# Kernel tuning notes

Hardware: AMD Instinct MI355X
Metric: run time of the kernel (lower is better)

## Reference

```python
import jax, jax.numpy as jnp
import numpy as np

NEG_SLOPE = 0.2
EPS = 1e-16  # PyG softmax denominator epsilon


def _gatv2_layer(x, src, dst, n_nodes, W_l, W_r, att, bias):
    """Single-head GATv2Conv (PyG defaults, self loops already in src/dst).
    x: [N, F_in]; src/dst: [E]; W_l/W_r: [F_in, F_out]; att: [F_out]; bias: [F_out].
    """
    x_l = x @ W_l                       # source transform [N, F_out]
    x_r = x @ W_r                       # target transform [N, F_out]
    # per-edge attention logit: a^T LeakyReLU(x_l[j] + x_r[i])
    e = jax.nn.leaky_relu(x_l[src] + x_r[dst], NEG_SLOPE) @ att  # [E]
    # softmax over incoming edges of each destination node
    e_max = jax.ops.segment_max(e, dst, num_segments=n_nodes)    # [N]
    ex = jnp.exp(e - e_max[dst])                                  # [E]
    denom = jax.ops.segment_sum(ex, dst, num_segments=n_nodes)   # [N]
    alpha = ex / (denom[dst] + EPS)                               # [E]
    out = jax.ops.segment_sum(alpha[:, None] * x_l[src], dst, num_segments=n_nodes)
    return out + bias


def setup_inputs() -> dict:
    key = jax.random.key(0)
    N, E = 50000, 800000
    IN, HID, OUT = 128, 64, 64
    ks = jax.random.split(key, 12)
    x = jax.random.normal(ks[0], (N, IN), dtype=jnp.float32)
    edge_index = jax.random.randint(ks[1], (2, E), 0, N, dtype=jnp.int64)
    s1 = float(1.0 / np.sqrt(IN))
    s2 = float(1.0 / np.sqrt(HID))
    return {
        "x": x,
        "edge_index": edge_index,
        "W1_l": jax.random.uniform(ks[2], (IN, HID), jnp.float32, -s1, s1),
        "W1_r": jax.random.uniform(ks[3], (IN, HID), jnp.float32, -s1, s1),
        "att1": jax.random.uniform(ks[4], (HID,), jnp.float32, -s2, s2),
        "b1": jnp.zeros((HID,), jnp.float32),
        "W2_l": jax.random.uniform(ks[5], (HID, OUT), jnp.float32, -s2, s2),
        "W2_r": jax.random.uniform(ks[6], (HID, OUT), jnp.float32, -s2, s2),
        "att2": jax.random.uniform(ks[7], (OUT,), jnp.float32, -s2, s2),
        "b2": jnp.zeros((OUT,), jnp.float32),
    }


def reference(x, edge_index, W1_l, W1_r, att1, b1, W2_l, W2_r, att2, b2):
    n = x.shape[0]
    loop = jnp.arange(n, dtype=edge_index.dtype)
    src = jnp.concatenate([edge_index[0], loop])  # add self loops (PyG default)
    dst = jnp.concatenate([edge_index[1], loop])
    h = _gatv2_layer(x, src, dst, n, W1_l, W1_r, att1, b1)
    h = jax.nn.relu(h)
    out = _gatv2_layer(h, src, dst, n, W2_l, W2_r, att2, b2)
    return out
```

## Files before the change

kernel.cpp:

```cpp
#include <hip/hip_runtime.h>
#include <math.h>

#define NEG_SLOPE 0.2f
#define EPSV 1e-16f
#define NEG_HUGE -1e30f
#define CAP 64
#define GH 512

typedef short short8 __attribute__((ext_vector_type(8)));
typedef float f32x4 __attribute__((ext_vector_type(4)));
typedef unsigned short u16;


__device__ __forceinline__ u16 f2bf(float f) {
    const unsigned u = __float_as_uint(f);
    return (u16)((u + 0x7fffu + ((u >> 16) & 1u)) >> 16);
}
__device__ __forceinline__ float bf2f(u16 h) {
    return __uint_as_float(((unsigned)h) << 16);
}

__global__ __launch_bounds__(256) void k_wpack(
        const float* __restrict__ W1l, const float* __restrict__ W1r,
        const float* __restrict__ W2l, const float* __restrict__ W2r,
        u16* __restrict__ w1hi, u16* __restrict__ w1lo,
        u16* __restrict__ w2hi, u16* __restrict__ w2lo,
        int* __restrict__ cnt, u16* __restrict__ csrc, int N, int NP) {
    const int idx = blockIdx.x * 256 + threadIdx.x;
    const int G = gridDim.x * 256;
    const int CN = 8 * NP;
    for (int i = idx; i < CN; i += G) {
        const int cls = i / NP;
        const int r = i - cls * NP;
        const int d = r * 8 + cls;
        cnt[i] = (d < N) ? 1 : 0;
    }
    for (int d = idx; d < N; d += G) csrc[(size_t)d * CAP] = (u16)d;
    const int T1 = 128 * 128, T2 = 64 * 128;
    if (idx >= T1 + T2) return;
    u16 *dhi, *dlo; const float *Wl, *Wr; int li;
    if (idx < T1) { dhi = w1hi; dlo = w1lo; Wl = W1l; Wr = W1r; li = idx; }
    else          { dhi = w2hi; dlo = w2lo; Wl = W2l; Wr = W2r; li = idx - T1; }
    const int j = li & 7, l = (li >> 3) & 63, t = (li >> 9) & 7, c = li >> 12;
    const int k = c * 32 + (l >> 4) * 8 + j;
    const int n = t * 16 + (l & 15);
    const float v = (n < 64) ? Wl[k * 64 + n] : Wr[k * 64 + (n - 64)];
    const unsigned u = __float_as_uint(v);
    dhi[li] = (u16)(u >> 16);
    const float hif = __uint_as_float(u & 0xffff0000u);
    dlo[li] = (u16)(__float_as_uint(v - hif) >> 16);
}

__device__ __forceinline__ void split8(const float* fs, short8& ahi, short8& alo) {
#pragma unroll
    for (int j = 0; j < 8; ++j) {
        const unsigned u = __float_as_uint(fs[j]);
        ahi[j] = (short)(u >> 16);
        const float hif = __uint_as_float(u & 0xffff0000u);
        alo[j] = (short)(__float_as_uint(fs[j] - hif) >> 16);
    }
}

template <int K>
__device__ __forceinline__ void gemm_mfma_tile(const float* __restrict__ X,
                                               const u16* __restrict__ whi,
                                               const u16* __restrict__ wlo,
                                               u16* __restrict__ xl,
                                               float* __restrict__ xr,
                                               int N, int tile) {
    const int lane = threadIdx.x & 63;
    const int w = threadIdx.x >> 6;
    const int rowbase = tile * 64 + w * 16;
    const int m = lane & 15, q = lane >> 4;
    int ar = rowbase + m; if (ar > N - 1) ar = N - 1;
    const float* arow = X + (size_t)ar * K + q * 8;
    f32x4 acc[8];
#pragma unroll
    for (int t = 0; t < 8; ++t) acc[t] = (f32x4){0.f, 0.f, 0.f, 0.f};
#pragma unroll
    for (int c = 0; c < K / 32; ++c) {
        const float4 f0 = *(const float4*)(arow + c * 32);
        const float4 f1 = *(const float4*)(arow + c * 32 + 4);
        const float fs[8] = {f0.x, f0.y, f0.z, f0.w, f1.x, f1.y, f1.z, f1.w};
        short8 ahi, alo;
        split8(fs, ahi, alo);
        const u16* bp = whi + ((size_t)(c * 8) * 64 + lane) * 8;
        const u16* bq = wlo + ((size_t)(c * 8) * 64 + lane) * 8;
#pragma unroll
        for (int t = 0; t < 8; ++t) {
            const short8 bhi = *(const short8*)(bp + t * 64 * 8);
            const short8 blo = *(const short8*)(bq + t * 64 * 8);
            acc[t] = __builtin_amdgcn_mfma_f32_16x16x32_bf16(bhi, ahi, acc[t], 0, 0, 0);
            acc[t] = __builtin_amdgcn_mfma_f32_16x16x32_bf16(blo, ahi, acc[t], 0, 0, 0);
            acc[t] = __builtin_amdgcn_mfma_f32_16x16x32_bf16(bhi, alo, acc[t], 0, 0, 0);
        }
    }
    const int row = rowbase + m;
    if (row < N) {
#pragma unroll
        for (int t = 0; t < 8; ++t) {
            const int colb = t * 16 + q * 4;
            if (t < 4) {
                ushort4 hv;
                hv.x = f2bf(acc[t][0]); hv.y = f2bf(acc[t][1]);
                hv.z = f2bf(acc[t][2]); hv.w = f2bf(acc[t][3]);
                *(ushort4*)(xl + (size_t)row * 64 + colb) = hv;
            } else {
                float4 v;
                v.x = acc[t][0]; v.y = acc[t][1]; v.z = acc[t][2]; v.w = acc[t][3];
                *(float4*)(xr + (size_t)row * 64 + (colb - 64)) = v;
            }
        }
    }
}

template <int K>
__global__ __launch_bounds__(256) void k_hist_gemm(const int* __restrict__ ei, int E,
                                                   int* __restrict__ cnt,
                                                   u16* __restrict__ csrc,
                                                   const float* __restrict__ X,
                                                   const u16* __restrict__ whi,
                                                   const u16* __restrict__ wlo,
                                                   u16* __restrict__ xl,
                                                   float* __restrict__ xr,
                                                   int N, int NP) {
    if ((int)blockIdx.x < GH) {
        const int cls = blockIdx.x & 7;
        const int stripe = blockIdx.x >> 3;
        const int NS = GH >> 3;
        const int tid = threadIdx.x;
        const int* srcp = ei;
        const int* dstp = ei + E;
        int* cntc = cnt + cls * NP;
        if ((E & 3) == 0) {
            for (int base = stripe * 1024; base < E; base += NS * 1024) {
                const int e4 = base + tid * 4;
                if (e4 < E) {
                    const int4 d4 = *(const int4*)(dstp + e4);
                    const int4 s4 = *(const int4*)(srcp + e4);
                    const int d[4] = {d4.x, d4.y, d4.z, d4.w};
                    const int s[4] = {s4.x, s4.y, s4.z, s4.w};
                    bool m[4]; int sl[4];
#pragma unroll
                    for (int j = 0; j < 4; ++j) {
                        m[j] = (d[j] & 7) == cls;
                        if (m[j]) sl[j] = atomicAdd(&cntc[d[j] >> 3], 1);
                    }
#pragma unroll
                    for (int j = 0; j < 4; ++j) {
                        if (m[j]) csrc[(size_t)d[j] * CAP + sl[j]] = (u16)s[j];
                    }
                }
            }
        } else {
            for (int base = stripe * 256; base < E; base += NS * 256) {
                const int e = base + tid;
                if (e < E) {
                    const int dd = dstp[e];
                    if ((dd & 7) == cls) {
                        const int ss = srcp[e];
                        const int slot = atomicAdd(&cntc[dd >> 3], 1);
                        csrc[(size_t)dd * CAP + slot] = (u16)ss;
                    }
                }
            }
        }
    } else {
        gemm_mfma_tile<K>(X, whi, wlo, xl, xr, N, blockIdx.x - GH);
    }
}

template <int K>
__global__ __launch_bounds__(256) void k_gemm(const float* __restrict__ X,
                                              const u16* __restrict__ whi,
                                              const u16* __restrict__ wlo,
                                              u16* __restrict__ xl,
                                              float* __restrict__ xr, int N) {
    gemm_mfma_tile<K>(X, whi, wlo, xl, xr, N, blockIdx.x);
}

template <int NT>
__device__ __forceinline__ void attn_core(const u16* __restrict__ xl,
                                          int sidx, int deg, int base,
                                          int g, int i,
                                          const float4 xrv, const float4 aw,
                                          float& l, float4& acc) {
    ushort4 u[NT][4];
    bool vv[NT][4];
#pragma unroll
    for (int nt = 0; nt < NT; ++nt) {
#pragma unroll
        for (int j = 0; j < 4; ++j) {
            const int s = base + nt * 16 + j * 4 + g;
            vv[nt][j] = s < deg;
            const int src = __shfl(sidx, s, 64);
            u[nt][j] = *(const ushort4*)(xl + (size_t)src * 64 + i * 4);
        }
    }
#pragma unroll
    for (int nt = 0; nt < NT; ++nt) {
#pragma unroll
        for (int j = 0; j < 4; ++j) {
            float4 va;
            va.x = bf2f(u[nt][j].x); va.y = bf2f(u[nt][j].y);
            va.z = bf2f(u[nt][j].z); va.w = bf2f(u[nt][j].w);
            float t0, pp;
            t0 = va.x + xrv.x; t0 = fmaxf(t0, NEG_SLOPE * t0); pp = aw.x * t0;
            t0 = va.y + xrv.y; t0 = fmaxf(t0, NEG_SLOPE * t0); pp = fmaf(aw.y, t0, pp);
            t0 = va.z + xrv.z; t0 = fmaxf(t0, NEG_SLOPE * t0); pp = fmaf(aw.z, t0, pp);
            t0 = va.w + xrv.w; t0 = fmaxf(t0, NEG_SLOPE * t0); pp = fmaf(aw.w, t0, pp);
            pp += __shfl_xor(pp, 1, 64);
            pp += __shfl_xor(pp, 2, 64);
            pp += __shfl_xor(pp, 4, 64);
            pp += __shfl_xor(pp, 8, 64);
            const float dj = __expf(vv[nt][j] ? pp : NEG_HUGE);
            l += dj;
            acc.x = fmaf(dj, va.x, acc.x);
            acc.y = fmaf(dj, va.y, acc.y);
            acc.z = fmaf(dj, va.z, acc.z);
            acc.w = fmaf(dj, va.w, acc.w);
        }
    }
}

__global__ __launch_bounds__(256) void k_attn(const u16* __restrict__ xl,
                                              const float* xr,
                                              const float* __restrict__ att,
                                              const int* __restrict__ cnt,
                                              const u16* __restrict__ csrc,
                                              const float* __restrict__ bias,
                                              float* out, int N, int NP, int relu) {
    const int lane = threadIdx.x & 63;
    const int g = lane >> 4;
    const int i = lane & 15;
    const int dst = blockIdx.x * 4 + (threadIdx.x >> 6);
    if (dst >= N) return;
    const float4 xrv = *(const float4*)(xr + (size_t)dst * 64 + i * 4);
    const float4 aw  = *(const float4*)(att + i * 4);
    const int deg = cnt[(dst & 7) * NP + (dst >> 3)];
    const int sidx = (int)csrc[(size_t)dst * CAP + ((lane < deg) ? lane : 0)];
    float l = 0.0f;
    float4 acc = {0.0f, 0.0f, 0.0f, 0.0f};
    if (deg <= 16) {
        attn_core<1>(xl, sidx, deg, 0, g, i, xrv, aw, l, acc);
    } else if (deg <= 32) {
        attn_core<2>(xl, sidx, deg, 0, g, i, xrv, aw, l, acc);
    } else {
        attn_core<2>(xl, sidx, deg, 0, g, i, xrv, aw, l, acc);
        attn_core<2>(xl, sidx, deg, 32, g, i, xrv, aw, l, acc);
    }
#pragma unroll
    for (int o = 16; o <= 32; o <<= 1) {
        l     += __shfl_xor(l, o, 64);
        acc.x += __shfl_xor(acc.x, o, 64);
        acc.y += __shfl_xor(acc.y, o, 64);
        acc.z += __shfl_xor(acc.z, o, 64);
        acc.w += __shfl_xor(acc.w, o, 64);
    }
    if (g == 0) {
        const float4 bv = *(const float4*)(bias + i * 4);
        const float inv = 1.0f / (l + EPSV);
        float4 r;
        r.x = fmaf(acc.x, inv, bv.x);
        r.y = fmaf(acc.y, inv, bv.y);
        r.z = fmaf(acc.z, inv, bv.z);
        r.w = fmaf(acc.w, inv, bv.w);
        if (relu) {
            r.x = fmaxf(r.x, 0.0f); r.y = fmaxf(r.y, 0.0f);
            r.z = fmaxf(r.z, 0.0f); r.w = fmaxf(r.w, 0.0f);
        }
        *(float4*)(out + (size_t)dst * 64 + i * 4) = r;
    }
}


extern "C" void kernel_launch(void* const* d_in, const int* in_sizes, int n_in,
                              void* d_out, int out_size, void* d_ws, size_t ws_size,
                              hipStream_t stream) {
    const float* x    = (const float*)d_in[0];
    const int*   ei   = (const int*)d_in[1];
    const float* W1l  = (const float*)d_in[2];
    const float* W1r  = (const float*)d_in[3];
    const float* att1 = (const float*)d_in[4];
    const float* b1   = (const float*)d_in[5];
    const float* W2l  = (const float*)d_in[6];
    const float* W2r  = (const float*)d_in[7];
    const float* att2 = (const float*)d_in[8];
    const float* b2   = (const float*)d_in[9];

    const int N  = in_sizes[0] / 128;
    const int E  = in_sizes[1] / 2;
    const int NP = (((N + 7) >> 3) + 31) & ~31;

    int* wsi   = (int*)d_ws;
    int* cnt   = wsi;
    u16* csrc  = (u16*)(cnt + 8 * NP);
    u16* w1hi  = csrc + (size_t)N * CAP;
    u16* w1lo  = w1hi + 16384;
    u16* w2hi  = w1lo + 16384;
    u16* w2lo  = w2hi + 8192;
    float* buf1 = (float*)(w2lo + 8192);
    float* buf2 = buf1 + (size_t)N * 64;
    float* fout = (float*)d_out;

    const dim3 b256(256);
    const int gGemm = (N + 63) / 64;
    const int gAttn = (N + 3) / 4;

    k_wpack<<<96, b256, 0, stream>>>(
        W1l, W1r, W2l, W2r, w1hi, w1lo, w2hi, w2lo, cnt, csrc, N, NP);

    k_hist_gemm<128><<<GH + gGemm, b256, 0, stream>>>(ei, E, cnt, csrc,
                                                      x, w1hi, w1lo,
                                                      (u16*)fout, buf1, N, NP);
    k_attn<<<gAttn, b256, 0, stream>>>((const u16*)fout, buf1, att1, cnt, csrc, b1,
                                       buf2, N, NP, 1);

    k_gemm<64><<<gGemm, b256, 0, stream>>>(buf2, w2hi, w2lo, (u16*)buf1, fout, N);
    k_attn<<<gAttn, b256, 0, stream>>>((const u16*)buf1, fout, att2, cnt, csrc, b2,
                                       fout, N, NP, 0);
}
```

Before: 206.9 us.

## Fuse layer-1 attention with layer-2 GEMM via shared-memory row tiles

Layer-1 attention and the layer-2 projection GEMM now run in one kernel. Each block computes 16 hidden rows into shared memory, then one wave multiplies them by W2 using split-bf16 MFMA and writes xl2/xr2 directly. This removes a kernel launch and the global round trip of the hidden activations. In exchange, only one of four waves does the GEMM while the others idle, and each wave now handles four destinations in sequence, which may cut memory-level parallelism in the gather phase.

```diff
diff --git a/kernel.cpp b/kernel.cpp
--- a/kernel.cpp
+++ b/kernel.cpp
@@ -170,15 +170,6 @@
     }
 }
 
-template <int K>
-__global__ __launch_bounds__(256) void k_gemm(const float* __restrict__ X,
-                                              const u16* __restrict__ whi,
-                                              const u16* __restrict__ wlo,
-                                              u16* __restrict__ xl,
-                                              float* __restrict__ xr, int N) {
-    gemm_mfma_tile<K>(X, whi, wlo, xl, xr, N, blockIdx.x);
-}
-
 template <int NT>
 __device__ __forceinline__ void attn_core(const u16* __restrict__ xl,
                                           int sidx, int deg, int base,
@@ -223,20 +214,15 @@
     }
 }
 
-__global__ __launch_bounds__(256) void k_attn(const u16* __restrict__ xl,
-                                              const float* xr,
-                                              const float* __restrict__ att,
-                                              const int* __restrict__ cnt,
-                                              const u16* __restrict__ csrc,
-                                              const float* __restrict__ bias,
-                                              float* out, int N, int NP, int relu) {
-    const int lane = threadIdx.x & 63;
-    const int g = lane >> 4;
-    const int i = lane & 15;
-    const int dst = blockIdx.x * 4 + (threadIdx.x >> 6);
-    if (dst >= N) return;
+__device__ __forceinline__ float4 attn_row(const u16* __restrict__ xl,
+                                           const float* __restrict__ xr,
+                                           const float4 aw,
+                                           const int* __restrict__ cnt,
+                                           const u16* __restrict__ csrc,
+                                           const float* __restrict__ bias,
+                                           int dst, int NP, int relu,
+                                           int lane, int g, int i) {
     const float4 xrv = *(const float4*)(xr + (size_t)dst * 64 + i * 4);
-    const float4 aw  = *(const float4*)(att + i * 4);
     const int deg = cnt[(dst & 7) * NP + (dst >> 3)];
     const int sidx = (int)csrc[(size_t)dst * CAP + ((lane < deg) ? lane : 0)];
     float l = 0.0f;
@@ -257,20 +243,103 @@
         acc.z += __shfl_xor(acc.z, o, 64);
         acc.w += __shfl_xor(acc.w, o, 64);
     }
-    if (g == 0) {
-        const float4 bv = *(const float4*)(bias + i * 4);
-        const float inv = 1.0f / (l + EPSV);
-        float4 r;
-        r.x = fmaf(acc.x, inv, bv.x);
-        r.y = fmaf(acc.y, inv, bv.y);
-        r.z = fmaf(acc.z, inv, bv.z);
-        r.w = fmaf(acc.w, inv, bv.w);
-        if (relu) {
-            r.x = fmaxf(r.x, 0.0f); r.y = fmaxf(r.y, 0.0f);
-            r.z = fmaxf(r.z, 0.0f); r.w = fmaxf(r.w, 0.0f);
-        }
+    const float4 bv = *(const float4*)(bias + i * 4);
+    const float inv = 1.0f / (l + EPSV);
+    float4 r;
+    r.x = fmaf(acc.x, inv, bv.x);
+    r.y = fmaf(acc.y, inv, bv.y);
+    r.z = fmaf(acc.z, inv, bv.z);
+    r.w = fmaf(acc.w, inv, bv.w);
+    if (relu) {
+        r.x = fmaxf(r.x, 0.0f); r.y = fmaxf(r.y, 0.0f);
+        r.z = fmaxf(r.z, 0.0f); r.w = fmaxf(r.w, 0.0f);
+    }
+    return r;
+}
+
+__global__ __launch_bounds__(256) void k_attn1_gemm2(
+        const u16* __restrict__ xl, const float* __restrict__ xr,
+        const float* __restrict__ att, const int* __restrict__ cnt,
+        const u16* __restrict__ csrc, const float* __restrict__ bias,
+        const u16* __restrict__ w2hi, const u16* __restrict__ w2lo,
+        u16* __restrict__ xl2, float* __restrict__ xr2, int N, int NP) {
+    __shared__ float hrow[16][68];
+    const int lane = threadIdx.x & 63;
+    const int wv = threadIdx.x >> 6;
+    const int g = lane >> 4;
+    const int i = lane & 15;
+    const int rowbase = blockIdx.x * 16;
+    const float4 aw = *(const float4*)(att + i * 4);
+    for (int p = 0; p < 4; ++p) {
+        const int dst = rowbase + wv * 4 + p;
+        if (dst < N) {
+            const float4 r = attn_row(xl, xr, aw, cnt, csrc, bias,
+                                      dst, NP, 1, lane, g, i);
+            if (g == 0) *(float4*)&hrow[wv * 4 + p][i * 4] = r;
+        }
+    }
+    __syncthreads();
+    if (wv != 0) return;
+    const int m = lane & 15, q = lane >> 4;
+    const float* arow = &hrow[m][0] + q * 8;
+    f32x4 acc[8];
+#pragma unroll
+    for (int t = 0; t < 8; ++t) acc[t] = (f32x4){0.f, 0.f, 0.f, 0.f};
+#pragma unroll
+    for (int c = 0; c < 2; ++c) {
+        const float4 f0 = *(const float4*)(arow + c * 32);
+        const float4 f1 = *(const float4*)(arow + c * 32 + 4);
+        const float fs[8] = {f0.x, f0.y, f0.z, f0.w, f1.x, f1.y, f1.z, f1.w};
+        short8 ahi, alo;
+        split8(fs, ahi, alo);
+        const u16* bp = w2hi + ((size_t)(c * 8) * 64 + lane) * 8;
+        const u16* bq = w2lo + ((size_t)(c * 8) * 64 + lane) * 8;
+#pragma unroll
+        for (int t = 0; t < 8; ++t) {
+            const short8 bhi = *(const short8*)(bp + t * 64 * 8);
+            const short8 blo = *(const short8*)(bq + t * 64 * 8);
+            acc[t] = __builtin_amdgcn_mfma_f32_16x16x32_bf16(bhi, ahi, acc[t], 0, 0, 0);
+            acc[t] = __builtin_amdgcn_mfma_f32_16x16x32_bf16(blo, ahi, acc[t], 0, 0, 0);
+            acc[t] = __builtin_amdgcn_mfma_f32_16x16x32_bf16(bhi, alo, acc[t], 0, 0, 0);
+        }
+    }
+    const int row = rowbase + m;
+    if (row < N) {
+#pragma unroll
+        for (int t = 0; t < 8; ++t) {
+            const int colb = t * 16 + q * 4;
+            if (t < 4) {
+                ushort4 hv;
+                hv.x = f2bf(acc[t][0]); hv.y = f2bf(acc[t][1]);
+                hv.z = f2bf(acc[t][2]); hv.w = f2bf(acc[t][3]);
+                *(ushort4*)(xl2 + (size_t)row * 64 + colb) = hv;
+            } else {
+                float4 v;
+                v.x = acc[t][0]; v.y = acc[t][1]; v.z = acc[t][2]; v.w = acc[t][3];
+                *(float4*)(xr2 + (size_t)row * 64 + (colb - 64)) = v;
+            }
+        }
+    }
+}
+
+__global__ __launch_bounds__(256) void k_attn(const u16* __restrict__ xl,
+                                              const float* __restrict__ xr,
+                                              const float* __restrict__ att,
+                                              const int* __restrict__ cnt,
+                                              const u16* __restrict__ csrc,
+                                              const float* __restrict__ bias,
+                                              float* __restrict__ out,
+                                              int N, int NP, int relu) {
+    const int lane = threadIdx.x & 63;
+    const int g = lane >> 4;
+    const int i = lane & 15;
+    const int dst = blockIdx.x * 4 + (threadIdx.x >> 6);
+    if (dst >= N) return;
+    const float4 aw = *(const float4*)(att + i * 4);
+    const float4 r = attn_row(xl, xr, aw, cnt, csrc, bias, dst, NP, relu,
+                              lane, g, i);
+    if (g == 0)
         *(float4*)(out + (size_t)dst * 64 + i * 4) = r;
-    }
 }
 
 
@@ -301,11 +370,13 @@
     u16* w2lo  = w2hi + 8192;
     float* buf1 = (float*)(w2lo + 8192);
     float* buf2 = buf1 + (size_t)N * 64;
+    float* buf3 = buf2 + (size_t)N * 64;
     float* fout = (float*)d_out;
 
     const dim3 b256(256);
     const int gGemm = (N + 63) / 64;
-    const int gAttn = (N + 3) / 4;
+    const int gA1   = (N + 15) / 16;
+    const int gA2   = (N + 3) / 4;
 
     k_wpack<<<96, b256, 0, stream>>>(
         W1l, W1r, W2l, W2r, w1hi, w1lo, w2hi, w2lo, cnt, csrc, N, NP);
@@ -313,10 +384,9 @@
     k_hist_gemm<128><<<GH + gGemm, b256, 0, stream>>>(ei, E, cnt, csrc,
                                                       x, w1hi, w1lo,
                                                       (u16*)fout, buf1, N, NP);
-    k_attn<<<gAttn, b256, 0, stream>>>((const u16*)fout, buf1, att1, cnt, csrc, b1,
-                                       buf2, N, NP, 1);
-
-    k_gemm<64><<<gGemm, b256, 0, stream>>>(buf2, w2hi, w2lo, (u16*)buf1, fout, N);
-    k_attn<<<gAttn, b256, 0, stream>>>((const u16*)buf1, fout, att2, cnt, csrc, b2,
-                                       fout, N, NP, 0);
-}
+    k_attn1_gemm2<<<gA1, b256, 0, stream>>>((const u16*)fout, buf1, att1,
+                                            cnt, csrc, b1, w2hi, w2lo,
+                                            (u16*)buf2, buf3, N, NP);
+    k_attn<<<gA2, b256, 0, stream>>>((const u16*)buf2, buf3, att2, cnt, csrc, b2,
+                                     fout, N, NP, 0);
+}
```

After: 231.3 us. 11.8% more time.
